# Kernel optimization log

Hardware: AMD Instinct MI355X
Metric: run time of the kernel (lower is better)

The kernel has to match this reference:

```python
import jax, jax.numpy as jnp
import numpy as np

D_IN = 1024
D_OUT = 1024
SEQ = 4096


def setup_inputs() -> dict:
    key = jax.random.key(0)
    kx, kq, kk, kv = jax.random.split(key, 4)
    s = 1.0 / np.sqrt(D_IN)
    return {
        "x": jax.random.normal(kx, (SEQ, D_IN), dtype=jnp.float32),
        # torch Linear weights: shape [d_out, d_in], y = x @ W.T
        "Wq": jax.random.uniform(kq, (D_OUT, D_IN), jnp.float32, -s, s),
        "Wk": jax.random.uniform(kk, (D_OUT, D_IN), jnp.float32, -s, s),
        "Wv": jax.random.uniform(kv, (D_OUT, D_IN), jnp.float32, -s, s),
    }


def reference(x, Wq, Wk, Wv):
    # QKV projections (no bias)
    q = x @ Wq.T  # [N, d_out]
    k = x @ Wk.T
    v = x @ Wv.T
    scale = 1.0 / jnp.sqrt(jnp.asarray(k.shape[-1], x.dtype))
    att = jax.nn.softmax((q @ k.T) * scale, axis=-1)  # [N, N]
    return att @ v  # [N, d_out]
```

## Files before the change

### kernel.cpp

```cpp
#include <hip/hip_runtime.h>
#include <hip/hip_bf16.h>
#include <math.h>

typedef __attribute__((ext_vector_type(8))) short short8;
typedef __attribute__((ext_vector_type(4))) float floatx4;

static __device__ __forceinline__ unsigned short f2bf(float f) {
    union { float f; unsigned int u; } a; a.f = f;
    unsigned int u = a.u;
    return (unsigned short)((u + 0x7FFFu + ((u >> 16) & 1u)) >> 16);
}

static __device__ __forceinline__ void cvt8(const float* __restrict__ src,
                                            unsigned short* __restrict__ dst, int i) {
    float4 v0 = *(const float4*)(src + i);
    float4 v1 = *(const float4*)(src + i + 4);
    ushort4 o0, o1;
    o0.x = f2bf(v0.x); o0.y = f2bf(v0.y); o0.z = f2bf(v0.z); o0.w = f2bf(v0.w);
    o1.x = f2bf(v1.x); o1.y = f2bf(v1.y); o1.z = f2bf(v1.z); o1.w = f2bf(v1.w);
    *(ushort4*)(dst + i) = o0;
    *(ushort4*)(dst + i + 4) = o1;
}

struct CV { const float* x; unsigned short* xb;
            const float* W[3]; unsigned short* Wb[3]; float* l; };
__global__ __launch_bounds__(256)
void cvt_all(CV a) {
    int b = blockIdx.x, t = threadIdx.x;
    if (b < 2048) {
        cvt8(a.x, a.xb, (b * 256 + t) * 8);
    } else if (b < 3584) {
        int z  = (b - 2048) >> 9;
        int bb = (b - 2048) & 511;
        cvt8(a.W[z], a.Wb[z], (bb * 256 + t) * 8);
    } else {
        float4 zz = {0.f, 0.f, 0.f, 0.f};
        #pragma unroll
        for (int c = 0; c < 4; c++)
            *(float4*)(a.l + t * 16 + c * 4) = zz;
    }
}

template<int BM, int BN, int BK, int TI, int TJ, int WCOLS>
__device__ __forceinline__ void gemm_core(const unsigned short* __restrict__ A,
                                          const unsigned short* __restrict__ B,
                                          int lda, int k_begin, int k_end,
                                          unsigned short* sA, unsigned short* sB,
                                          floatx4 (&acc)[TI][TJ],
                                          int bm, int bn)
{
    constexpr int CPR = BK / 8;
    constexpr int RPR = 2048 / BK;
    const int t    = threadIdx.x;
    const int wave = t >> 6;
    const int lane = t & 63;
    const int wm = (wave / WCOLS) * (TI * 16);
    const int wn = (wave % WCOLS) * (TJ * 16);

    const int srow   = t / CPR;
    const int schunk = t % CPR;
    const int gchunk = schunk ^ (srow & (CPR - 1));
    const int lm  = lane & 15;
    const int swz = lm & (CPR - 1);

    for (int k0 = k_begin; k0 < k_end; k0 += BK) {
        __syncthreads();
        #pragma unroll
        for (int r = 0; r < (BM * BK) / 2048; r++) {
            const unsigned short* gA =
                A + (size_t)(bm + srow + r * RPR) * lda + k0 + gchunk * 8;
            __builtin_amdgcn_global_load_lds(
                (const __attribute__((address_space(1))) void*)gA,
                (__attribute__((address_space(3))) void*)((char*)sA + wave * 1024 + r * 4096),
                16, 0, 0);
        }
        #pragma unroll
        for (int r = 0; r < (BN * BK) / 2048; r++) {
            const unsigned short* gB =
                B + (size_t)(bn + srow + r * RPR) * lda + k0 + gchunk * 8;
            __builtin_amdgcn_global_load_lds(
                (const __attribute__((address_space(1))) void*)gB,
                (__attribute__((address_space(3))) void*)((char*)sB + wave * 1024 + r * 4096),
                16, 0, 0);
        }
        __syncthreads();

        #pragma unroll
        for (int kk = 0; kk < BK; kk += 32) {
            const int c  = (kk >> 3) + (lane >> 4);
            const int ce = ((c ^ swz) << 3);
            short8 a_frag[TI], b_frag[TJ];
            #pragma unroll
            for (int i = 0; i < TI; i++)
                a_frag[i] = *(const short8*)&sA[(wm + i * 16 + lm) * BK + ce];
            #pragma unroll
            for (int j = 0; j < TJ; j++)
                b_frag[j] = *(const short8*)&sB[(wn + j * 16 + lm) * BK + ce];
            #pragma unroll
            for (int i = 0; i < TI; i++)
                #pragma unroll
                for (int j = 0; j < TJ; j++)
                    acc[i][j] = __builtin_amdgcn_mfma_f32_16x16x32_bf16(
                        a_frag[i], b_frag[j], acc[i][j], 0, 0, 0);
        }
    }
}


struct P3 { const unsigned short* W[3]; unsigned short* O[3]; };
__global__ __launch_bounds__(256)
void proj3(const unsigned short* __restrict__ xb, P3 a) {
    __shared__ unsigned short sA[128 * 64];
    __shared__ unsigned short sB[128 * 64];
    const int z = blockIdx.z;
    const unsigned short* B = a.W[z];
    unsigned short* O = a.O[z];
    const bool trans = (z == 2);
    const int ldc = trans ? 4096 : 1024;
    const float scale = (z == 0) ? 0.03125f : 1.0f;

    floatx4 acc[4][4];
    #pragma unroll
    for (int i = 0; i < 4; i++)
        #pragma unroll
        for (int j = 0; j < 4; j++) { floatx4 zz = {0.f,0.f,0.f,0.f}; acc[i][j] = zz; }

    const int bm = blockIdx.y * 128, bn = blockIdx.x * 128;
    gemm_core<128, 128, 64, 4, 4, 2>(xb, B, 1024, 0, 1024, sA, sB, acc, bm, bn);

    const int lane = threadIdx.x & 63, wave = threadIdx.x >> 6;
    const int wm = (wave >> 1) * 64, wn = (wave & 1) * 64;
    const int lm = lane & 15, rq = (lane >> 4) * 4;
    #pragma unroll
    for (int i = 0; i < 4; i++)
        #pragma unroll
        for (int j = 0; j < 4; j++) {
            int tm = bm + wm + i * 16 + rq;
            int tn = bn + wn + j * 16 + lm;
            #pragma unroll
            for (int r = 0; r < 4; r++) {
                unsigned short h = f2bf(acc[i][j][r] * scale);
                size_t idx = trans ? ((size_t)tn * ldc + (tm + r))
                                   : ((size_t)(tm + r) * ldc + tn);
                O[idx] = h;
            }
        }
}

__global__ __launch_bounds__(256)
void gemm_ps(const unsigned short* __restrict__ q, const unsigned short* __restrict__ k,
             unsigned short* __restrict__ Pm, float* __restrict__ l) {
    __shared__ unsigned short sA[128 * 128];
    __shared__ unsigned short sB[128 * 128];

    const int lid = blockIdx.x;
    const int xcd = lid & 7;
    const int i8  = lid >> 3;
    const int by  = (xcd & 1) * 16 + (i8 & 15);
    const int bx  = (xcd >> 1) * 8 + (i8 >> 4);

    floatx4 acc[4][4];
    #pragma unroll
    for (int i = 0; i < 4; i++)
        #pragma unroll
        for (int j = 0; j < 4; j++) { floatx4 zz = {0.f,0.f,0.f,0.f}; acc[i][j] = zz; }

    const int bm = by * 128, bn = bx * 128;
    gemm_core<128, 128, 128, 4, 4, 2>(q, k, 1024, 0, 1024, sA, sB, acc, bm, bn);

    const int lane = threadIdx.x & 63, wave = threadIdx.x >> 6;
    const int wm = (wave >> 1) * 64, wn = (wave & 1) * 64;
    const int lm = lane & 15, rq = (lane >> 4) * 4;
    #pragma unroll
    for (int i = 0; i < 4; i++) {
        #pragma unroll
        for (int r = 0; r < 4; r++) {
            int row = bm + wm + i * 16 + rq + r;
            float rs = 0.f;
            #pragma unroll
            for (int j = 0; j < 4; j++) {
                float e = __expf(acc[i][j][r]);
                rs += e;
                int tn = bn + wn + j * 16 + lm;
                Pm[(size_t)row * 4096 + tn] = f2bf(e);
            }
            rs += __shfl_xor(rs, 1);
            rs += __shfl_xor(rs, 2);
            rs += __shfl_xor(rs, 4);
            rs += __shfl_xor(rs, 8);
            if (lm == 0) atomicAdd(l + row, rs);
        }
    }
}

__global__ __launch_bounds__(256)
void gemm_osplit(const unsigned short* __restrict__ Pm, const unsigned short* __restrict__ vT,
                 float* __restrict__ Opart) {
    __shared__ unsigned short sA[128 * 128];
    __shared__ unsigned short sB[128 * 128];

    const int lid = blockIdx.x;
    const int xcd = lid & 7;
    const int w   = lid >> 6;
    const int g   = (lid >> 3) & 7;
    const int s   = w * 8 + xcd;
    const int z   = s >> 5;
    const int row = s & 31;

    floatx4 acc[4][4];
    #pragma unroll
    for (int i = 0; i < 4; i++)
        #pragma unroll
        for (int j = 0; j < 4; j++) { floatx4 zz = {0.f,0.f,0.f,0.f}; acc[i][j] = zz; }

    const int bm = row * 128, bn = g * 128;
    gemm_core<128, 128, 128, 4, 4, 2>(Pm, vT, 4096, z * 2048, (z + 1) * 2048,
                                      sA, sB, acc, bm, bn);

    float* Op = Opart + (size_t)z * (4096 * 1024);
    const int lane = threadIdx.x & 63, wave = threadIdx.x >> 6;
    const int wm = (wave >> 1) * 64, wn = (wave & 1) * 64;
    const int lm = lane & 15, rq = (lane >> 4) * 4;
    #pragma unroll
    for (int i = 0; i < 4; i++)
        #pragma unroll
        for (int j = 0; j < 4; j++) {
            int tm = bm + wm + i * 16 + rq;
            int tn = bn + wn + j * 16 + lm;
            #pragma unroll
            for (int r = 0; r < 4; r++)
                Op[(size_t)(tm + r) * 1024 + tn] = acc[i][j][r];
        }
}

__global__ __launch_bounds__(256)
void reduce_scale(const float* __restrict__ Op, const float* __restrict__ l,
                  float* __restrict__ out) {
    int i = (blockIdx.x * 256 + threadIdx.x) * 4;
    float4 a = *(const float4*)(Op + i);
    float4 b = *(const float4*)(Op + 4096 * 1024 + i);
    float inv = 1.0f / l[i >> 10];
    float4 o;
    o.x = (a.x + b.x) * inv; o.y = (a.y + b.y) * inv;
    o.z = (a.z + b.z) * inv; o.w = (a.w + b.w) * inv;
    *(float4*)(out + i) = o;
}

extern "C" void kernel_launch(void* const* d_in, const int* in_sizes, int n_in,
                              void* d_out, int out_size, void* d_ws, size_t ws_size,
                              hipStream_t stream) {
    const float* x  = (const float*)d_in[0];
    const float* Wq = (const float*)d_in[1];
    const float* Wk = (const float*)d_in[2];
    const float* Wv = (const float*)d_in[3];
    float* out = (float*)d_out;

    const int SEQ = 4096, D = 1024;
    char* ws = (char*)d_ws;
    const size_t MB = 1u << 20;
    unsigned short* vTb = (unsigned short*)(ws);
    unsigned short* xb  = (unsigned short*)(ws + 8 * MB);
    unsigned short* Wqb = (unsigned short*)(ws + 16 * MB);
    unsigned short* Wkb = (unsigned short*)(ws + 18 * MB);
    unsigned short* Wvb = (unsigned short*)(ws + 20 * MB);
    unsigned short* qb  = (unsigned short*)(ws + 22 * MB);
    unsigned short* kb  = (unsigned short*)(ws + 30 * MB);
    unsigned short* P   = (unsigned short*)(ws + 38 * MB);
    float*          l   = (float*)(ws + 70 * MB);
    float*          Opart = (float*)(ws + 72 * MB);

    dim3 blk(256);
    CV cv = {x, xb, {Wq, Wk, Wv}, {Wqb, Wkb, Wvb}, l};
    cvt_all<<<dim3(3585), blk, 0, stream>>>(cv);

    P3 p3 = {{Wqb, Wkb, Wvb}, {qb, kb, vTb}};
    proj3<<<dim3(D / 128, SEQ / 128, 3), blk, 0, stream>>>(xb, p3);

    gemm_ps<<<dim3(1024), blk, 0, stream>>>(qb, kb, P, l);

    gemm_osplit<<<dim3(512), blk, 0, stream>>>(P, vTb, Opart);

    reduce_scale<<<(SEQ * D) / 1024, blk, 0, stream>>>(Opart, l, out);
}
```

Measured before the change: 219.3 us.

## Store split-K partials in bf16, widen proj3 K-tile, remap blocks per XCD, vectorize vT store

The split-K partial outputs of the PV GEMM are now written and read as bf16 instead of fp32, which halves that intermediate traffic at the cost of extra rounding before the final sum. The projection kernel moves to a 1D grid with an XCD-aware block-to-tile mapping and a 128-wide K tile. The transposed V store is vectorized into ushort4 writes. Together these aim to cut memory traffic and improve cache locality across XCDs, while increasing LDS use per block in proj3.

```diff
diff --git a/kernel.cpp b/kernel.cpp
--- a/kernel.cpp
+++ b/kernel.cpp
@@ -9,6 +9,10 @@
     union { float f; unsigned int u; } a; a.f = f;
     unsigned int u = a.u;
     return (unsigned short)((u + 0x7FFFu + ((u >> 16) & 1u)) >> 16);
+}
+static __device__ __forceinline__ float bf2f(unsigned short h) {
+    union { unsigned int u; float f; } a; a.u = ((unsigned int)h) << 16;
+    return a.f;
 }
 
 static __device__ __forceinline__ void cvt8(const float* __restrict__ src,
@@ -110,13 +114,19 @@
 struct P3 { const unsigned short* W[3]; unsigned short* O[3]; };
 __global__ __launch_bounds__(256)
 void proj3(const unsigned short* __restrict__ xb, P3 a) {
-    __shared__ unsigned short sA[128 * 64];
-    __shared__ unsigned short sB[128 * 64];
-    const int z = blockIdx.z;
+    __shared__ unsigned short sA[128 * 128];
+    __shared__ unsigned short sB[128 * 128];
+
+    const int lid = blockIdx.x;
+    const int xcd = lid & 7;
+    const int rem = lid >> 3;
+    const int row = (rem & 7) * 4 + (xcd >> 1);
+    const int col = ((rem >> 3) & 3) * 2 + (xcd & 1);
+    const int z   = rem >> 5;
+
     const unsigned short* B = a.W[z];
     unsigned short* O = a.O[z];
     const bool trans = (z == 2);
-    const int ldc = trans ? 4096 : 1024;
     const float scale = (z == 0) ? 0.03125f : 1.0f;
 
     floatx4 acc[4][4];
@@ -125,8 +135,8 @@
         #pragma unroll
         for (int j = 0; j < 4; j++) { floatx4 zz = {0.f,0.f,0.f,0.f}; acc[i][j] = zz; }
 
-    const int bm = blockIdx.y * 128, bn = blockIdx.x * 128;
-    gemm_core<128, 128, 64, 4, 4, 2>(xb, B, 1024, 0, 1024, sA, sB, acc, bm, bn);
+    const int bm = row * 128, bn = col * 128;
+    gemm_core<128, 128, 128, 4, 4, 2>(xb, B, 1024, 0, 1024, sA, sB, acc, bm, bn);
 
     const int lane = threadIdx.x & 63, wave = threadIdx.x >> 6;
     const int wm = (wave >> 1) * 64, wn = (wave & 1) * 64;
@@ -137,12 +147,17 @@
         for (int j = 0; j < 4; j++) {
             int tm = bm + wm + i * 16 + rq;
             int tn = bn + wn + j * 16 + lm;
-            #pragma unroll
-            for (int r = 0; r < 4; r++) {
-                unsigned short h = f2bf(acc[i][j][r] * scale);
-                size_t idx = trans ? ((size_t)tn * ldc + (tm + r))
-                                   : ((size_t)(tm + r) * ldc + tn);
-                O[idx] = h;
+            if (trans) {
+                ushort4 h4;
+                h4.x = f2bf(acc[i][j][0]);
+                h4.y = f2bf(acc[i][j][1]);
+                h4.z = f2bf(acc[i][j][2]);
+                h4.w = f2bf(acc[i][j][3]);
+                *(ushort4*)&O[(size_t)tn * 4096 + tm] = h4;
+            } else {
+                #pragma unroll
+                for (int r = 0; r < 4; r++)
+                    O[(size_t)(tm + r) * 1024 + tn] = f2bf(acc[i][j][r] * scale);
             }
         }
 }
@@ -195,7 +210,7 @@
 
 __global__ __launch_bounds__(256)
 void gemm_osplit(const unsigned short* __restrict__ Pm, const unsigned short* __restrict__ vT,
-                 float* __restrict__ Opart) {
+                 unsigned short* __restrict__ Opart) {
     __shared__ unsigned short sA[128 * 128];
     __shared__ unsigned short sB[128 * 128];
 
@@ -217,7 +232,7 @@
     gemm_core<128, 128, 128, 4, 4, 2>(Pm, vT, 4096, z * 2048, (z + 1) * 2048,
                                       sA, sB, acc, bm, bn);
 
-    float* Op = Opart + (size_t)z * (4096 * 1024);
+    unsigned short* Op = Opart + (size_t)z * (4096 * 1024);
     const int lane = threadIdx.x & 63, wave = threadIdx.x >> 6;
     const int wm = (wave >> 1) * 64, wn = (wave & 1) * 64;
     const int lm = lane & 15, rq = (lane >> 4) * 4;
@@ -229,20 +244,22 @@
             int tn = bn + wn + j * 16 + lm;
             #pragma unroll
             for (int r = 0; r < 4; r++)
-                Op[(size_t)(tm + r) * 1024 + tn] = acc[i][j][r];
-        }
-}
-
-__global__ __launch_bounds__(256)
-void reduce_scale(const float* __restrict__ Op, const float* __restrict__ l,
+                Op[(size_t)(tm + r) * 1024 + tn] = f2bf(acc[i][j][r]);
+        }
+}
+
+__global__ __launch_bounds__(256)
+void reduce_scale(const unsigned short* __restrict__ Op, const float* __restrict__ l,
                   float* __restrict__ out) {
     int i = (blockIdx.x * 256 + threadIdx.x) * 4;
-    float4 a = *(const float4*)(Op + i);
-    float4 b = *(const float4*)(Op + 4096 * 1024 + i);
+    ushort4 a = *(const ushort4*)(Op + i);
+    ushort4 b = *(const ushort4*)(Op + 4096 * 1024 + i);
     float inv = 1.0f / l[i >> 10];
     float4 o;
-    o.x = (a.x + b.x) * inv; o.y = (a.y + b.y) * inv;
-    o.z = (a.z + b.z) * inv; o.w = (a.w + b.w) * inv;
+    o.x = (bf2f(a.x) + bf2f(b.x)) * inv;
+    o.y = (bf2f(a.y) + bf2f(b.y)) * inv;
+    o.z = (bf2f(a.z) + bf2f(b.z)) * inv;
+    o.w = (bf2f(a.w) + bf2f(b.w)) * inv;
     *(float4*)(out + i) = o;
 }
 
@@ -267,14 +284,14 @@
     unsigned short* kb  = (unsigned short*)(ws + 30 * MB);
     unsigned short* P   = (unsigned short*)(ws + 38 * MB);
     float*          l   = (float*)(ws + 70 * MB);
-    float*          Opart = (float*)(ws + 72 * MB);
+    unsigned short* Opart = (unsigned short*)(ws + 72 * MB);
 
     dim3 blk(256);
     CV cv = {x, xb, {Wq, Wk, Wv}, {Wqb, Wkb, Wvb}, l};
     cvt_all<<<dim3(3585), blk, 0, stream>>>(cv);
 
     P3 p3 = {{Wqb, Wkb, Wvb}, {qb, kb, vTb}};
-    proj3<<<dim3(D / 128, SEQ / 128, 3), blk, 0, stream>>>(xb, p3);
+    proj3<<<dim3(768), blk, 0, stream>>>(xb, p3);
 
     gemm_ps<<<dim3(1024), blk, 0, stream>>>(qb, kb, P, l);
 
```

Measured after the change: 200.3 us. 1.1x faster.
